# Performance work log

Measured on AMD Instinct MI355X. Metric: run time of the kernel, lower is better.

The kernel has to match this reference:

```python
import jax, jax.numpy as jnp
import numpy as np

H = 256   # hidden_size
B = 64    # batch_size
LP = 2048 # passage length
LQ = 64   # question length


def _linear(x, W, b):
    # torch nn.Linear: y = x @ W.T + b
    return jnp.matmul(x, W.T) + b


def _gru_cell(x, h, w_ih, w_hh, b_ih, b_hh):
    # torch GRUCell semantics: x is input, h is hidden state
    gi = jnp.matmul(x, w_ih.T) + b_ih   # [B, 3*2H]
    gh = jnp.matmul(h, w_hh.T) + b_hh
    i_r, i_z, i_n = jnp.split(gi, 3, axis=-1)
    h_r, h_z, h_n = jnp.split(gh, 3, axis=-1)
    r = jax.nn.sigmoid(i_r + h_r)
    z = jax.nn.sigmoid(i_z + h_z)
    n = jnp.tanh(i_n + r * h_n)
    return (1.0 - z) * n + z * h


def setup_inputs() -> dict:
    key = jax.random.key(0)
    ks = jax.random.split(key, 17)
    s = lambda i, shape: jax.random.normal(ks[i], shape, dtype=jnp.float32) * 0.05
    return {
        "passEnc": jax.random.normal(ks[0], (LP, B, 2 * H), dtype=jnp.float32),
        "quesEnc": jax.random.normal(ks[1], (LQ, B, 2 * H), dtype=jnp.float32),
        "WQu_W": s(2, (H, 2 * H)), "WQu_b": s(3, (H,)),
        "WQv_W": s(4, (H, H)),     "WQv_b": s(5, (H,)),
        "WPh_W": s(6, (H, 2 * H)), "WPh_b": s(7, (H,)),
        "Wah_W": s(8, (H, 2 * H)), "Wah_b": s(9, (H,)),
        "Vt1": s(10, (B, H, 1)),
        "Vt2": s(11, (B, H, 1)),
        "VQr": s(12, (1, 1, H)),
        "gru_wih": s(13, (6 * H, 2 * H)), "gru_whh": s(14, (6 * H, 2 * H)),
        "gru_bih": s(15, (6 * H,)),       "gru_bhh": s(16, (6 * H,)),
    }


def reference(passEnc, quesEnc, WQu_W, WQu_b, WQv_W, WQv_b, WPh_W, WPh_b,
              Wah_W, Wah_b, Vt1, Vt2, VQr, gru_wih, gru_whh, gru_bih, gru_bhh):
    # --- question-aware initial state rQ ---
    # temp: [lQ, B, H] (VQr path broadcasts over lQ and B)
    temp = jnp.tanh(_linear(quesEnc, WQu_W, WQu_b) + _linear(VQr, WQv_W, WQv_b))
    sQ = jnp.einsum('qbh,bh->bq', temp, Vt1[..., 0])          # [B, lQ]
    a = jax.nn.softmax(sQ, axis=1)
    rQ = jnp.einsum('bq,qbd->bd', a, quesEnc)                 # [B, 2H]

    passP = _linear(passEnc, WPh_W, WPh_b)                    # [lP, B, H], reused both steps

    def pointer_step(rQ):
        temp2 = jnp.tanh(passP + _linear(rQ, Wah_W, Wah_b))   # [lP, B, H]
        sP = jnp.einsum('pbh,bh->bp', temp2, Vt2[..., 0])     # [B, lP]
        aP = jax.nn.softmax(sP, axis=1)
        ct = jnp.einsum('bp,pbd->bd', aP, passEnc)            # [B, 2H]
        return aP, ct

    aP1, ct = pointer_step(rQ)
    rQ = _gru_cell(rQ, ct, gru_wih, gru_whh, gru_bih, gru_bhh)
    aP2, _ = pointer_step(rQ)
    return (aP1, aP2)


if __name__ == "__main__":
    out = reference(**setup_inputs())
    print(out[0].shape, out[1].shape)
```

## Files before the change

kernel.cpp:

```cpp
#include <hip/hip_runtime.h>
#include <math.h>


constexpr int Bn   = 64;
constexpr int Hn   = 256;
constexpr int D2H  = 512;
constexpr int LPn  = 2048;
constexpr int LQn  = 64;

typedef __attribute__((ext_vector_type(8))) short bf16x8;
typedef __attribute__((ext_vector_type(4))) float f32x4;
typedef __attribute__((ext_vector_type(4))) short short4v;

__device__ inline float waveAllSum(float v) {
  #pragma unroll
  for (int o = 32; o > 0; o >>= 1) v += __shfl_xor(v, o, 64);
  return v;
}
__device__ inline float waveAllMax(float v) {
  #pragma unroll
  for (int o = 32; o > 0; o >>= 1) v = fmaxf(v, __shfl_xor(v, o, 64));
  return v;
}

__device__ inline short f2bf(float f) {
  union { float f; unsigned u; } v; v.f = f;
  unsigned r = v.u + 0x7FFF + ((v.u >> 16) & 1);
  return (short)(r >> 16);
}

__global__ __launch_bounds__(256) void k_wcvt(const float* __restrict__ WQu,
                                              const float* __restrict__ WPh,
                                              short* __restrict__ wqu16,
                                              short* __restrict__ wph16) {
  int e = (blockIdx.x * 256 + threadIdx.x) * 4;
  const float* src; short* dst; int off;
  if (e < 131072) { src = WQu; dst = wqu16; off = e; }
  else            { src = WPh; dst = wph16; off = e - 131072; }
  f32x4 f = *(const f32x4*)&src[off];
  short4v h;
  h[0] = f2bf(f[0]); h[1] = f2bf(f[1]); h[2] = f2bf(f[2]); h[3] = f2bf(f[3]);
  *(short4v*)&dst[off] = h;
}

__global__ __launch_bounds__(256) void k_v2(const float* __restrict__ VQr,
                                            const float* __restrict__ WQv_W,
                                            const float* __restrict__ WQv_b,
                                            float* __restrict__ v2) {
  __shared__ float s[256];
  int t = threadIdx.x;
  s[t] = VQr[t];
  __syncthreads();
  float acc = WQv_b[t];
  for (int k = 0; k < 256; ++k) acc += s[k] * WQv_W[t * 256 + k];
  v2[t] = acc;
}

__global__ __launch_bounds__(256) void k_mfma_fused(
    const float* __restrict__ A,
    const short* __restrict__ Wb,
    const float* __restrict__ bias,
    const float* __restrict__ u,
    const float* __restrict__ vt,
    float* __restrict__ C,
    float* __restrict__ sOut,
    int ustride, int sstride)
{
  __shared__ __align__(16) short Abuf[64 * 72];
  __shared__ __align__(16) short Bbuf[256 * 72];
  __shared__ float sred[4][64];

  const int tid  = threadIdx.x;
  const int w    = tid >> 6;
  const int l    = tid & 63;
  const int l15  = l & 15;
  const int quad = l >> 4;
  const long bm  = (long)blockIdx.x * 64;

  f32x4 acc[4][4];
  #pragma unroll
  for (int i = 0; i < 4; ++i)
    #pragma unroll
    for (int j = 0; j < 4; ++j)
      acc[i][j] = (f32x4)0.f;

  for (int k0 = 0; k0 < 512; k0 += 64) {
    {
      const int r  = tid >> 2;
      const int ks = (tid & 3) * 16;
      const f32x4* src = (const f32x4*)&A[(bm + r) * 512 + k0 + ks];
      f32x4 f0 = src[0], f1 = src[1], f2 = src[2], f3 = src[3];
      bf16x8 h0, h1;
      h0[0] = f2bf(f0[0]); h0[1] = f2bf(f0[1]); h0[2] = f2bf(f0[2]); h0[3] = f2bf(f0[3]);
      h0[4] = f2bf(f1[0]); h0[5] = f2bf(f1[1]); h0[6] = f2bf(f1[2]); h0[7] = f2bf(f1[3]);
      h1[0] = f2bf(f2[0]); h1[1] = f2bf(f2[1]); h1[2] = f2bf(f2[2]); h1[3] = f2bf(f2[3]);
      h1[4] = f2bf(f3[0]); h1[5] = f2bf(f3[1]); h1[6] = f2bf(f3[2]); h1[7] = f2bf(f3[3]);
      *(bf16x8*)&Abuf[r * 72 + ks]     = h0;
      *(bf16x8*)&Abuf[r * 72 + ks + 8] = h1;
    }
    #pragma unroll
    for (int q = 0; q < 8; ++q) {
      int n = q * 32 + (tid >> 3);
      int s = tid & 7;
      bf16x8 vsh = *(const bf16x8*)&Wb[n * 512 + k0 + s * 8];
      *(bf16x8*)&Bbuf[n * 72 + s * 8] = vsh;
    }
    __syncthreads();
    #pragma unroll
    for (int h = 0; h < 2; ++h) {
      bf16x8 af[4], bfr[4];
      #pragma unroll
      for (int i = 0; i < 4; ++i)
        af[i] = *(const bf16x8*)&Abuf[(i * 16 + l15) * 72 + h * 32 + quad * 8];
      #pragma unroll
      for (int j = 0; j < 4; ++j)
        bfr[j] = *(const bf16x8*)&Bbuf[(w * 64 + j * 16 + l15) * 72 + h * 32 + quad * 8];
      #pragma unroll
      for (int i = 0; i < 4; ++i)
        #pragma unroll
        for (int j = 0; j < 4; ++j)
          acc[i][j] = __builtin_amdgcn_mfma_f32_16x16x32_bf16(af[i], bfr[j], acc[i][j], 0, 0, 0);
    }
    __syncthreads();
  }

  float srow[4][4];
  #pragma unroll
  for (int i = 0; i < 4; ++i) {
    #pragma unroll
    for (int r = 0; r < 4; ++r) {
      const int row = i * 16 + quad * 4 + r;
      float s_acc = 0.f;
      #pragma unroll
      for (int j = 0; j < 4; ++j) {
        const int n = w * 64 + j * 16 + l15;
        float val = acc[i][j][r] + bias[n];
        if (C) C[(bm + row) * 256 + n] = val;
        float uu = u[ustride * row + n];
        s_acc += tanhf(val + uu) * vt[row * 256 + n];
      }
      srow[i][r] = s_acc;
    }
  }
  #pragma unroll
  for (int off = 1; off < 16; off <<= 1) {
    #pragma unroll
    for (int i = 0; i < 4; ++i)
      #pragma unroll
      for (int r = 0; r < 4; ++r)
        srow[i][r] += __shfl_xor(srow[i][r], off, 64);
  }
  if (l15 == 0) {
    #pragma unroll
    for (int i = 0; i < 4; ++i)
      #pragma unroll
      for (int r = 0; r < 4; ++r)
        sred[w][i * 16 + quad * 4 + r] = srow[i][r];
  }
  __syncthreads();
  if (tid < 64) {
    float s = sred[0][tid] + sred[1][tid] + sred[2][tid] + sred[3][tid];
    sOut[(long)tid * sstride + blockIdx.x] = s;
  }
}

constexpr int TM = 64, TN = 64, TK = 32;
constexpr int PAD = 4;

__global__ __launch_bounds__(256) void k_gemm(const float* __restrict__ A,
                                              const float* __restrict__ W,
                                              const float* __restrict__ bias,
                                              float* __restrict__ C,
                                              int M, int N, int K) {
  __shared__ float As[TK][TM + PAD];
  __shared__ float Bs[TK][TN + PAD];
  const int bm = blockIdx.x * TM;
  const int bn = blockIdx.y * TN;
  const int tid = threadIdx.x;
  const int tx = tid & 15;
  const int ty = tid >> 4;
  float acc[4][4] = {};

  for (int k0 = 0; k0 < K; k0 += TK) {
    #pragma unroll
    for (int i = 0; i < 2; ++i) {
      int f = tid + 256 * i;
      int m = f >> 3;
      int kq = (f & 7) << 2;
      float4 v = *(const float4*)&A[(size_t)(bm + m) * K + k0 + kq];
      As[kq + 0][m] = v.x; As[kq + 1][m] = v.y; As[kq + 2][m] = v.z; As[kq + 3][m] = v.w;
    }
    #pragma unroll
    for (int i = 0; i < 2; ++i) {
      int f = tid + 256 * i;
      int n = f >> 3;
      int kq = (f & 7) << 2;
      float4 v = *(const float4*)&W[(size_t)(bn + n) * K + k0 + kq];
      Bs[kq + 0][n] = v.x; Bs[kq + 1][n] = v.y; Bs[kq + 2][n] = v.z; Bs[kq + 3][n] = v.w;
    }
    __syncthreads();
    #pragma unroll
    for (int k = 0; k < TK; ++k) {
      float4 a4 = *(const float4*)&As[k][ty * 4];
      float4 b4 = *(const float4*)&Bs[k][tx * 4];
      float aa[4] = {a4.x, a4.y, a4.z, a4.w};
      float bb[4] = {b4.x, b4.y, b4.z, b4.w};
      #pragma unroll
      for (int i = 0; i < 4; ++i)
        #pragma unroll
        for (int j = 0; j < 4; ++j)
          acc[i][j] = fmaf(aa[i], bb[j], acc[i][j]);
    }
    __syncthreads();
  }

  float4 bset = *(const float4*)&bias[bn + tx * 4];
  #pragma unroll
  for (int i = 0; i < 4; ++i) {
    int m = bm + ty * 4 + i;
    float4 v;
    v.x = acc[i][0] + bset.x;
    v.y = acc[i][1] + bset.y;
    v.z = acc[i][2] + bset.z;
    v.w = acc[i][3] + bset.w;
    *(float4*)&C[(size_t)m * N + bn + tx * 4] = v;
  }
}

__global__ __launch_bounds__(256) void k_softmax_rq(const float* __restrict__ sQ,
                                                    const float* __restrict__ quesEnc,
                                                    float* __restrict__ rQ) {
  int b = blockIdx.x, tid = threadIdx.x;
  __shared__ float s_a[LQn];
  if (tid < 64) {
    float s = sQ[b * LQn + tid];
    float m = waveAllMax(s);
    float e = expf(s - m);
    float sum = waveAllSum(e);
    s_a[tid] = e / sum;
  }
  __syncthreads();
  #pragma unroll
  for (int rep = 0; rep < 2; ++rep) {
    int d = tid + rep * 256;
    float acc = 0.f;
    for (int q = 0; q < LQn; ++q)
      acc += s_a[q] * quesEnc[(size_t)(q * Bn + b) * D2H + d];
    rQ[b * D2H + d] = acc;
  }
}

__global__ __launch_bounds__(256) void k_sp(const float* __restrict__ passP,
                                            const float* __restrict__ u,
                                            const float* __restrict__ Vt2,
                                            float* __restrict__ sP) {
  int flat = blockIdx.x * 4 + (threadIdx.x >> 6);
  int lane = threadIdx.x & 63;
  int b = flat & (Bn - 1);
  int p = flat >> 6;
  float4 v  = *(const float4*)&passP[(size_t)flat * Hn + lane * 4];
  float4 uu = *(const float4*)&u[b * Hn + lane * 4];
  float4 vt = *(const float4*)&Vt2[b * Hn + lane * 4];
  float s = tanhf(v.x + uu.x) * vt.x + tanhf(v.y + uu.y) * vt.y +
            tanhf(v.z + uu.z) * vt.z + tanhf(v.w + uu.w) * vt.w;
  s = waveAllSum(s);
  if (lane == 0) sP[b * LPn + p] = s;
}

__global__ __launch_bounds__(256) void k_softmax(const float* __restrict__ sP,
                                                 float* __restrict__ out) {
  int b = blockIdx.x, tid = threadIdx.x;
  int lane = tid & 63, wid = tid >> 6;
  __shared__ float red[4];
  float v[8];
  float m = -1e30f;
  #pragma unroll
  for (int i = 0; i < 8; ++i) {
    v[i] = sP[b * LPn + i * 256 + tid];
    m = fmaxf(m, v[i]);
  }
  m = waveAllMax(m);
  if (lane == 0) red[wid] = m;
  __syncthreads();
  m = fmaxf(fmaxf(red[0], red[1]), fmaxf(red[2], red[3]));
  float s = 0.f;
  #pragma unroll
  for (int i = 0; i < 8; ++i) { v[i] = expf(v[i] - m); s += v[i]; }
  s = waveAllSum(s);
  __syncthreads();
  if (lane == 0) red[wid] = s;
  __syncthreads();
  s = red[0] + red[1] + red[2] + red[3];
  float inv = 1.0f / s;
  #pragma unroll
  for (int i = 0; i < 8; ++i) out[b * LPn + i * 256 + tid] = v[i] * inv;
}

__global__ __launch_bounds__(256) void k_ct(const float* __restrict__ aP,
                                            const float* __restrict__ passEnc,
                                            float* __restrict__ ct) {
  int b = blockIdx.x;
  int p0 = blockIdx.y * 64;
  int tid = threadIdx.x;
  float acc0 = 0.f, acc1 = 0.f;
  for (int pp = 0; pp < 64; ++pp) {
    int p = p0 + pp;
    float a = aP[b * LPn + p];
    const float* row = &passEnc[(size_t)(p * Bn + b) * D2H];
    acc0 += a * row[tid];
    acc1 += a * row[tid + 256];
  }
  atomicAdd(&ct[b * D2H + tid], acc0);
  atomicAdd(&ct[b * D2H + tid + 256], acc1);
}

__global__ __launch_bounds__(256) void k_gates(const float* __restrict__ gi,
                                               const float* __restrict__ gh,
                                               const float* __restrict__ ct,
                                               float* __restrict__ rQ2) {
  int idx = blockIdx.x * 256 + threadIdx.x;
  int b = idx >> 9;
  int j = idx & 511;
  const float* gib = gi + b * 1536;
  const float* ghb = gh + b * 1536;
  float r = 1.f / (1.f + expf(-(gib[j] + ghb[j])));
  float z = 1.f / (1.f + expf(-(gib[512 + j] + ghb[512 + j])));
  float n = tanhf(gib[1024 + j] + r * ghb[1024 + j]);
  rQ2[b * D2H + j] = (1.f - z) * n + z * ct[b * D2H + j];
}

extern "C" void kernel_launch(void* const* d_in, const int* in_sizes, int n_in,
                              void* d_out, int out_size, void* d_ws, size_t ws_size,
                              hipStream_t stream) {
  const float* passEnc  = (const float*)d_in[0];
  const float* quesEnc  = (const float*)d_in[1];
  const float* WQu_W    = (const float*)d_in[2];
  const float* WQu_b    = (const float*)d_in[3];
  const float* WQv_W    = (const float*)d_in[4];
  const float* WQv_b    = (const float*)d_in[5];
  const float* WPh_W    = (const float*)d_in[6];
  const float* WPh_b    = (const float*)d_in[7];
  const float* Wah_W    = (const float*)d_in[8];
  const float* Wah_b    = (const float*)d_in[9];
  const float* Vt1      = (const float*)d_in[10];
  const float* Vt2      = (const float*)d_in[11];
  const float* VQr      = (const float*)d_in[12];
  const float* gru_wih  = (const float*)d_in[13];
  const float* gru_whh  = (const float*)d_in[14];
  const float* gru_bih  = (const float*)d_in[15];
  const float* gru_bhh  = (const float*)d_in[16];
  float* out = (float*)d_out;

  float* ws = (float*)d_ws;
  float* passP = ws;
  float* v2    = ws + 33554432;
  float* rQ    = v2 + 256;
  float* u1    = rQ + 32768;
  float* u2    = u1 + 16384;
  float* sP    = u2 + 16384;
  float* ct    = sP + 131072;
  float* gi    = ct + 32768;
  float* gh    = gi + 98304;
  float* rQ2   = gh + 98304;
  float* sQ    = rQ2 + 32768;
  short* wqu16 = (short*)(sQ + 4096);
  short* wph16 = wqu16 + 131072;

  k_wcvt<<<256, 256, 0, stream>>>(WQu_W, WPh_W, wqu16, wph16);

  k_v2<<<1, 256, 0, stream>>>(VQr, WQv_W, WQv_b, v2);
  k_mfma_fused<<<LQn, 256, 0, stream>>>(quesEnc, wqu16, WQu_b, v2, Vt1,
                                        nullptr, sQ, 0, LQn);
  k_softmax_rq<<<Bn, 256, 0, stream>>>(sQ, quesEnc, rQ);
  k_gemm<<<dim3(1, Hn / TN), 256, 0, stream>>>(rQ, Wah_W, Wah_b, u1, Bn, Hn, D2H);

  k_mfma_fused<<<LPn, 256, 0, stream>>>(passEnc, wph16, WPh_b, u1, Vt2,
                                        passP, sP, Hn, LPn);
  k_softmax<<<Bn, 256, 0, stream>>>(sP, out);

  hipMemsetAsync(ct, 0, Bn * D2H * sizeof(float), stream);
  k_ct<<<dim3(Bn, LPn / 64), 256, 0, stream>>>(out, passEnc, ct);

  k_gemm<<<dim3(1, 1536 / TN), 256, 0, stream>>>(rQ, gru_wih, gru_bih, gi, Bn, 1536, D2H);
  k_gemm<<<dim3(1, 1536 / TN), 256, 0, stream>>>(ct, gru_whh, gru_bhh, gh, Bn, 1536, D2H);
  k_gates<<<Bn * D2H / 256, 256, 0, stream>>>(gi, gh, ct, rQ2);

  k_gemm<<<dim3(1, Hn / TN), 256, 0, stream>>>(rQ2, Wah_W, Wah_b, u2, Bn, Hn, D2H);
  k_sp<<<LPn * Bn / 4, 256, 0, stream>>>(passP, u2, Vt2, sP);
  k_softmax<<<Bn, 256, 0, stream>>>(sP, out + Bn * LPn);
}
```

Measured before the change: 907.0 us.

## Pre-swizzle weights for direct MFMA loads, fuse GRU and small GEMMs, vectorize ct

Weights are converted into an MFMA-fragment-ordered bf16 layout so the main fused GEMM reads A and B operands straight from global memory into registers, with no LDS staging or barriers, and runs at a 3-waves occupancy hint. The rQ softmax is fused with the u1 projection, and the two GRU GEMMs are fused with the gates into one kernel. A separate small GEMV kernel computes u2. The ct reduction is vectorized with fewer atomics. This removes several launches and LDS traffic, at the cost of uncoalesced-per-row GEMV weight reads and of losing LDS reuse of A and B in the big GEMM.

```diff
diff --git a/kernel.cpp b/kernel.cpp
--- a/kernel.cpp
+++ b/kernel.cpp
@@ -10,7 +10,6 @@
 
 typedef __attribute__((ext_vector_type(8))) short bf16x8;
 typedef __attribute__((ext_vector_type(4))) float f32x4;
-typedef __attribute__((ext_vector_type(4))) short short4v;
 
 __device__ inline float waveAllSum(float v) {
   #pragma unroll
@@ -23,24 +22,49 @@
   return v;
 }
 
-__device__ inline short f2bf(float f) {
+__device__ inline short f2bf_rtne(float f) {
   union { float f; unsigned u; } v; v.f = f;
   unsigned r = v.u + 0x7FFF + ((v.u >> 16) & 1);
   return (short)(r >> 16);
 }
 
+__device__ inline unsigned pk2(float lo, float hi) {
+  union { float f; unsigned u; } a, b; a.f = lo; b.f = hi;
+  return __builtin_amdgcn_perm(b.u + 0x8000u, a.u + 0x8000u, 0x07060302u);
+}
+__device__ inline bf16x8 cvt8(f32x4 a0, f32x4 a1) {
+  union { unsigned u[4]; bf16x8 v; } r;
+  r.u[0] = pk2(a0[0], a0[1]);
+  r.u[1] = pk2(a0[2], a0[3]);
+  r.u[2] = pk2(a1[0], a1[1]);
+  r.u[3] = pk2(a1[2], a1[3]);
+  return r.v;
+}
+
 __global__ __launch_bounds__(256) void k_wcvt(const float* __restrict__ WQu,
                                               const float* __restrict__ WPh,
-                                              short* __restrict__ wqu16,
-                                              short* __restrict__ wph16) {
-  int e = (blockIdx.x * 256 + threadIdx.x) * 4;
-  const float* src; short* dst; int off;
-  if (e < 131072) { src = WQu; dst = wqu16; off = e; }
-  else            { src = WPh; dst = wph16; off = e - 131072; }
-  f32x4 f = *(const f32x4*)&src[off];
-  short4v h;
-  h[0] = f2bf(f[0]); h[1] = f2bf(f[1]); h[2] = f2bf(f[2]); h[3] = f2bf(f[3]);
-  *(short4v*)&dst[off] = h;
+                                              short* __restrict__ q2,
+                                              short* __restrict__ p2) {
+  int s = blockIdx.x * 256 + threadIdx.x;
+  const float* W; short* D; int slot;
+  if (s < 16384) { W = WQu; D = q2; slot = s; }
+  else           { W = WPh; D = p2; slot = s - 16384; }
+  int l    = slot & 63;
+  int rest = slot >> 6;
+  int h    = rest & 1;
+  int k0i  = (rest >> 1) & 7;
+  int wj   = rest >> 4;
+  int l15  = l & 15, quad = l >> 4;
+  int n = (wj >> 2) * 64 + (wj & 3) * 16 + l15;
+  int k = k0i * 64 + h * 32 + quad * 8;
+  f32x4 f0 = *(const f32x4*)&W[n * 512 + k];
+  f32x4 f1 = *(const f32x4*)&W[n * 512 + k + 4];
+  bf16x8 o;
+  o[0] = f2bf_rtne(f0[0]); o[1] = f2bf_rtne(f0[1]);
+  o[2] = f2bf_rtne(f0[2]); o[3] = f2bf_rtne(f0[3]);
+  o[4] = f2bf_rtne(f1[0]); o[5] = f2bf_rtne(f1[1]);
+  o[6] = f2bf_rtne(f1[2]); o[7] = f2bf_rtne(f1[3]);
+  *(bf16x8*)&D[slot * 8] = o;
 }
 
 __global__ __launch_bounds__(256) void k_v2(const float* __restrict__ VQr,
@@ -56,9 +80,9 @@
   v2[t] = acc;
 }
 
-__global__ __launch_bounds__(256) void k_mfma_fused(
+__global__ __launch_bounds__(256, 3) void k_mfma_fused(
     const float* __restrict__ A,
-    const short* __restrict__ Wb,
+    const short* __restrict__ Wb2,
     const float* __restrict__ bias,
     const float* __restrict__ u,
     const float* __restrict__ vt,
@@ -66,10 +90,7 @@
     float* __restrict__ sOut,
     int ustride, int sstride)
 {
-  __shared__ __align__(16) short Abuf[64 * 72];
-  __shared__ __align__(16) short Bbuf[256 * 72];
   __shared__ float sred[4][64];
-
   const int tid  = threadIdx.x;
   const int w    = tid >> 6;
   const int l    = tid & 63;
@@ -84,44 +105,40 @@
     for (int j = 0; j < 4; ++j)
       acc[i][j] = (f32x4)0.f;
 
-  for (int k0 = 0; k0 < 512; k0 += 64) {
-    {
-      const int r  = tid >> 2;
-      const int ks = (tid & 3) * 16;
-      const f32x4* src = (const f32x4*)&A[(bm + r) * 512 + k0 + ks];
-      f32x4 f0 = src[0], f1 = src[1], f2 = src[2], f3 = src[3];
-      bf16x8 h0, h1;
-      h0[0] = f2bf(f0[0]); h0[1] = f2bf(f0[1]); h0[2] = f2bf(f0[2]); h0[3] = f2bf(f0[3]);
-      h0[4] = f2bf(f1[0]); h0[5] = f2bf(f1[1]); h0[6] = f2bf(f1[2]); h0[7] = f2bf(f1[3]);
-      h1[0] = f2bf(f2[0]); h1[1] = f2bf(f2[1]); h1[2] = f2bf(f2[2]); h1[3] = f2bf(f2[3]);
-      h1[4] = f2bf(f3[0]); h1[5] = f2bf(f3[1]); h1[6] = f2bf(f3[2]); h1[7] = f2bf(f3[3]);
-      *(bf16x8*)&Abuf[r * 72 + ks]     = h0;
-      *(bf16x8*)&Abuf[r * 72 + ks + 8] = h1;
-    }
-    #pragma unroll
-    for (int q = 0; q < 8; ++q) {
-      int n = q * 32 + (tid >> 3);
-      int s = tid & 7;
-      bf16x8 vsh = *(const bf16x8*)&Wb[n * 512 + k0 + s * 8];
-      *(bf16x8*)&Bbuf[n * 72 + s * 8] = vsh;
-    }
-    __syncthreads();
+  const float* arow[4];
+  #pragma unroll
+  for (int i = 0; i < 4; ++i)
+    arow[i] = A + (size_t)(bm + i * 16 + l15) * 512 + quad * 8;
+  const short* bptr = Wb2 + (size_t)w * 4 * 8192 + l * 8;
+
+  for (int k0i = 0; k0i < 8; ++k0i) {
+    const int k0 = k0i * 64;
+    f32x4 a0[4][2], a1[4][2];
+    #pragma unroll
+    for (int i = 0; i < 4; ++i)
+      #pragma unroll
+      for (int h = 0; h < 2; ++h) {
+        const float* p = arow[i] + k0 + h * 32;
+        a0[i][h] = *(const f32x4*)p;
+        a1[i][h] = *(const f32x4*)(p + 4);
+      }
+    bf16x8 bfr[2][4];
+    #pragma unroll
+    for (int h = 0; h < 2; ++h)
+      #pragma unroll
+      for (int j = 0; j < 4; ++j)
+        bfr[h][j] = *(const bf16x8*)(bptr + j * 8192 + k0i * 1024 + h * 512);
     #pragma unroll
     for (int h = 0; h < 2; ++h) {
-      bf16x8 af[4], bfr[4];
-      #pragma unroll
-      for (int i = 0; i < 4; ++i)
-        af[i] = *(const bf16x8*)&Abuf[(i * 16 + l15) * 72 + h * 32 + quad * 8];
-      #pragma unroll
-      for (int j = 0; j < 4; ++j)
-        bfr[j] = *(const bf16x8*)&Bbuf[(w * 64 + j * 16 + l15) * 72 + h * 32 + quad * 8];
+      bf16x8 af[4];
+      #pragma unroll
+      for (int i = 0; i < 4; ++i) af[i] = cvt8(a0[i][h], a1[i][h]);
       #pragma unroll
       for (int i = 0; i < 4; ++i)
         #pragma unroll
         for (int j = 0; j < 4; ++j)
-          acc[i][j] = __builtin_amdgcn_mfma_f32_16x16x32_bf16(af[i], bfr[j], acc[i][j], 0, 0, 0);
+          acc[i][j] = __builtin_amdgcn_mfma_f32_16x16x32_bf16(af[i], bfr[h][j], acc[i][j], 0, 0, 0);
     }
-    __syncthreads();
   }
 
   float srow[4][4];
@@ -136,102 +153,39 @@
         const int n = w * 64 + j * 16 + l15;
         float val = acc[i][j][r] + bias[n];
         if (C) C[(bm + row) * 256 + n] = val;
-        float uu = u[ustride * row + n];
-        s_acc += tanhf(val + uu) * vt[row * 256 + n];
+        s_acc += tanhf(val + u[ustride * row + n]) * vt[row * 256 + n];
       }
       srow[i][r] = s_acc;
     }
   }
   #pragma unroll
-  for (int off = 1; off < 16; off <<= 1) {
+  for (int off = 1; off < 16; off <<= 1)
     #pragma unroll
     for (int i = 0; i < 4; ++i)
       #pragma unroll
       for (int r = 0; r < 4; ++r)
         srow[i][r] += __shfl_xor(srow[i][r], off, 64);
-  }
-  if (l15 == 0) {
+  if (l15 == 0)
     #pragma unroll
     for (int i = 0; i < 4; ++i)
       #pragma unroll
       for (int r = 0; r < 4; ++r)
         sred[w][i * 16 + quad * 4 + r] = srow[i][r];
-  }
-  __syncthreads();
-  if (tid < 64) {
-    float s = sred[0][tid] + sred[1][tid] + sred[2][tid] + sred[3][tid];
-    sOut[(long)tid * sstride + blockIdx.x] = s;
-  }
-}
-
-constexpr int TM = 64, TN = 64, TK = 32;
-constexpr int PAD = 4;
-
-__global__ __launch_bounds__(256) void k_gemm(const float* __restrict__ A,
-                                              const float* __restrict__ W,
-                                              const float* __restrict__ bias,
-                                              float* __restrict__ C,
-                                              int M, int N, int K) {
-  __shared__ float As[TK][TM + PAD];
-  __shared__ float Bs[TK][TN + PAD];
-  const int bm = blockIdx.x * TM;
-  const int bn = blockIdx.y * TN;
-  const int tid = threadIdx.x;
-  const int tx = tid & 15;
-  const int ty = tid >> 4;
-  float acc[4][4] = {};
-
-  for (int k0 = 0; k0 < K; k0 += TK) {
-    #pragma unroll
-    for (int i = 0; i < 2; ++i) {
-      int f = tid + 256 * i;
-      int m = f >> 3;
-      int kq = (f & 7) << 2;
-      float4 v = *(const float4*)&A[(size_t)(bm + m) * K + k0 + kq];
-      As[kq + 0][m] = v.x; As[kq + 1][m] = v.y; As[kq + 2][m] = v.z; As[kq + 3][m] = v.w;
-    }
-    #pragma unroll
-    for (int i = 0; i < 2; ++i) {
-      int f = tid + 256 * i;
-      int n = f >> 3;
-      int kq = (f & 7) << 2;
-      float4 v = *(const float4*)&W[(size_t)(bn + n) * K + k0 + kq];
-      Bs[kq + 0][n] = v.x; Bs[kq + 1][n] = v.y; Bs[kq + 2][n] = v.z; Bs[kq + 3][n] = v.w;
-    }
-    __syncthreads();
-    #pragma unroll
-    for (int k = 0; k < TK; ++k) {
-      float4 a4 = *(const float4*)&As[k][ty * 4];
-      float4 b4 = *(const float4*)&Bs[k][tx * 4];
-      float aa[4] = {a4.x, a4.y, a4.z, a4.w};
-      float bb[4] = {b4.x, b4.y, b4.z, b4.w};
-      #pragma unroll
-      for (int i = 0; i < 4; ++i)
-        #pragma unroll
-        for (int j = 0; j < 4; ++j)
-          acc[i][j] = fmaf(aa[i], bb[j], acc[i][j]);
-    }
-    __syncthreads();
-  }
-
-  float4 bset = *(const float4*)&bias[bn + tx * 4];
-  #pragma unroll
-  for (int i = 0; i < 4; ++i) {
-    int m = bm + ty * 4 + i;
-    float4 v;
-    v.x = acc[i][0] + bset.x;
-    v.y = acc[i][1] + bset.y;
-    v.z = acc[i][2] + bset.z;
-    v.w = acc[i][3] + bset.w;
-    *(float4*)&C[(size_t)m * N + bn + tx * 4] = v;
-  }
-}
-
-__global__ __launch_bounds__(256) void k_softmax_rq(const float* __restrict__ sQ,
-                                                    const float* __restrict__ quesEnc,
-                                                    float* __restrict__ rQ) {
+  __syncthreads();
+  if (tid < 64)
+    sOut[(size_t)tid * sstride + blockIdx.x] =
+        sred[0][tid] + sred[1][tid] + sred[2][tid] + sred[3][tid];
+}
+
+__global__ __launch_bounds__(256) void k_rq_u1(const float* __restrict__ sQ,
+                                               const float* __restrict__ quesEnc,
+                                               const float* __restrict__ Wah,
+                                               const float* __restrict__ Wah_b,
+                                               float* __restrict__ rQ,
+                                               float* __restrict__ u1) {
   int b = blockIdx.x, tid = threadIdx.x;
   __shared__ float s_a[LQn];
+  __shared__ float s_r[D2H];
   if (tid < 64) {
     float s = sQ[b * LQn + tid];
     float m = waveAllMax(s);
@@ -246,8 +200,18 @@
     float acc = 0.f;
     for (int q = 0; q < LQn; ++q)
       acc += s_a[q] * quesEnc[(size_t)(q * Bn + b) * D2H + d];
+    s_r[d] = acc;
     rQ[b * D2H + d] = acc;
   }
+  __syncthreads();
+  float accu = Wah_b[tid];
+  const float* wr = Wah + (size_t)tid * 512;
+  for (int k4 = 0; k4 < 128; ++k4) {
+    f32x4 wv = *(const f32x4*)&wr[k4 * 4];
+    f32x4 rv = *(const f32x4*)&s_r[k4 * 4];
+    accu += wv[0] * rv[0] + wv[1] * rv[1] + wv[2] * rv[2] + wv[3] * rv[3];
+  }
+  u1[b * Hn + tid] = accu;
 }
 
 __global__ __launch_bounds__(256) void k_sp(const float* __restrict__ passP,
@@ -299,34 +263,89 @@
 __global__ __launch_bounds__(256) void k_ct(const float* __restrict__ aP,
                                             const float* __restrict__ passEnc,
                                             float* __restrict__ ct) {
-  int b = blockIdx.x;
-  int p0 = blockIdx.y * 64;
-  int tid = threadIdx.x;
-  float acc0 = 0.f, acc1 = 0.f;
+  int b = blockIdx.x, pc = blockIdx.y, tid = threadIdx.x;
+  int dg = tid & 127;
+  int pg = tid >> 7;
+  f32x4 acc = (f32x4)0.f;
   for (int pp = 0; pp < 64; ++pp) {
-    int p = p0 + pp;
+    int p = pc * 128 + pg * 64 + pp;
     float a = aP[b * LPn + p];
-    const float* row = &passEnc[(size_t)(p * Bn + b) * D2H];
-    acc0 += a * row[tid];
-    acc1 += a * row[tid + 256];
-  }
-  atomicAdd(&ct[b * D2H + tid], acc0);
-  atomicAdd(&ct[b * D2H + tid + 256], acc1);
-}
-
-__global__ __launch_bounds__(256) void k_gates(const float* __restrict__ gi,
-                                               const float* __restrict__ gh,
-                                               const float* __restrict__ ct,
-                                               float* __restrict__ rQ2) {
-  int idx = blockIdx.x * 256 + threadIdx.x;
-  int b = idx >> 9;
-  int j = idx & 511;
-  const float* gib = gi + b * 1536;
-  const float* ghb = gh + b * 1536;
-  float r = 1.f / (1.f + expf(-(gib[j] + ghb[j])));
-  float z = 1.f / (1.f + expf(-(gib[512 + j] + ghb[512 + j])));
-  float n = tanhf(gib[1024 + j] + r * ghb[1024 + j]);
-  rQ2[b * D2H + j] = (1.f - z) * n + z * ct[b * D2H + j];
+    acc += a * *(const f32x4*)&passEnc[((size_t)p * Bn + b) * D2H + dg * 4];
+  }
+  __shared__ f32x4 sacc[256];
+  sacc[tid] = acc;
+  __syncthreads();
+  if (pg == 0) {
+    acc += sacc[tid + 128];
+    float* dst = &ct[b * D2H + dg * 4];
+    atomicAdd(dst + 0, acc[0]);
+    atomicAdd(dst + 1, acc[1]);
+    atomicAdd(dst + 2, acc[2]);
+    atomicAdd(dst + 3, acc[3]);
+  }
+}
+
+__global__ __launch_bounds__(256) void k_gru(const float* __restrict__ rQ,
+                                             const float* __restrict__ ct,
+                                             const float* __restrict__ wih,
+                                             const float* __restrict__ whh,
+                                             const float* __restrict__ bih,
+                                             const float* __restrict__ bhh,
+                                             float* __restrict__ rQ2) {
+  int m = blockIdx.x;
+  int j = blockIdx.y * 256 + threadIdx.x;
+  __shared__ float sx[D2H], sh[D2H];
+  sx[threadIdx.x]       = rQ[m * D2H + threadIdx.x];
+  sx[threadIdx.x + 256] = rQ[m * D2H + threadIdx.x + 256];
+  sh[threadIdx.x]       = ct[m * D2H + threadIdx.x];
+  sh[threadIdx.x + 256] = ct[m * D2H + threadIdx.x + 256];
+  __syncthreads();
+  float gr = bih[j], gz = bih[512 + j], gn = bih[1024 + j];
+  float hr = bhh[j], hz = bhh[512 + j], hn = bhh[1024 + j];
+  const float* wr0 = wih + (size_t)j * 512;
+  const float* wr1 = wih + (size_t)(512 + j) * 512;
+  const float* wr2 = wih + (size_t)(1024 + j) * 512;
+  const float* vr0 = whh + (size_t)j * 512;
+  const float* vr1 = whh + (size_t)(512 + j) * 512;
+  const float* vr2 = whh + (size_t)(1024 + j) * 512;
+  for (int k4 = 0; k4 < 128; ++k4) {
+    f32x4 x = *(const f32x4*)&sx[k4 * 4];
+    f32x4 h = *(const f32x4*)&sh[k4 * 4];
+    f32x4 w0 = *(const f32x4*)&wr0[k4 * 4];
+    f32x4 w1 = *(const f32x4*)&wr1[k4 * 4];
+    f32x4 w2 = *(const f32x4*)&wr2[k4 * 4];
+    f32x4 v0 = *(const f32x4*)&vr0[k4 * 4];
+    f32x4 v1 = *(const f32x4*)&vr1[k4 * 4];
+    f32x4 v2 = *(const f32x4*)&vr2[k4 * 4];
+    #pragma unroll
+    for (int e = 0; e < 4; ++e) {
+      gr += w0[e] * x[e]; gz += w1[e] * x[e]; gn += w2[e] * x[e];
+      hr += v0[e] * h[e]; hz += v1[e] * h[e]; hn += v2[e] * h[e];
+    }
+  }
+  float r = 1.f / (1.f + expf(-(gr + hr)));
+  float z = 1.f / (1.f + expf(-(gz + hz)));
+  float nn = tanhf(gn + r * hn);
+  rQ2[m * D2H + j] = (1.f - z) * nn + z * sh[j];
+}
+
+__global__ __launch_bounds__(256) void k_u2(const float* __restrict__ rQ2,
+                                            const float* __restrict__ Wah,
+                                            const float* __restrict__ Wah_b,
+                                            float* __restrict__ u2) {
+  int m = blockIdx.x, n = threadIdx.x;
+  __shared__ float s_r[D2H];
+  s_r[n]       = rQ2[m * D2H + n];
+  s_r[n + 256] = rQ2[m * D2H + n + 256];
+  __syncthreads();
+  float acc = Wah_b[n];
+  const float* wr = Wah + (size_t)n * 512;
+  for (int k4 = 0; k4 < 128; ++k4) {
+    f32x4 wv = *(const f32x4*)&wr[k4 * 4];
+    f32x4 rv = *(const f32x4*)&s_r[k4 * 4];
+    acc += wv[0] * rv[0] + wv[1] * rv[1] + wv[2] * rv[2] + wv[3] * rv[3];
+  }
+  u2[m * Hn + n] = acc;
 }
 
 extern "C" void kernel_launch(void* const* d_in, const int* in_sizes, int n_in,
@@ -359,33 +378,29 @@
   float* u2    = u1 + 16384;
   float* sP    = u2 + 16384;
   float* ct    = sP + 131072;
-  float* gi    = ct + 32768;
-  float* gh    = gi + 98304;
-  float* rQ2   = gh + 98304;
+  float* rQ2   = ct + 32768;
   float* sQ    = rQ2 + 32768;
-  short* wqu16 = (short*)(sQ + 4096);
-  short* wph16 = wqu16 + 131072;
-
-  k_wcvt<<<256, 256, 0, stream>>>(WQu_W, WPh_W, wqu16, wph16);
-
+  short* wqu2  = (short*)(sQ + 4096);
+  short* wph2  = wqu2 + 131072;
+
+  k_wcvt<<<128, 256, 0, stream>>>(WQu_W, WPh_W, wqu2, wph2);
   k_v2<<<1, 256, 0, stream>>>(VQr, WQv_W, WQv_b, v2);
-  k_mfma_fused<<<LQn, 256, 0, stream>>>(quesEnc, wqu16, WQu_b, v2, Vt1,
+
+  k_mfma_fused<<<LQn, 256, 0, stream>>>(quesEnc, wqu2, WQu_b, v2, Vt1,
                                         nullptr, sQ, 0, LQn);
-  k_softmax_rq<<<Bn, 256, 0, stream>>>(sQ, quesEnc, rQ);
-  k_gemm<<<dim3(1, Hn / TN), 256, 0, stream>>>(rQ, Wah_W, Wah_b, u1, Bn, Hn, D2H);
-
-  k_mfma_fused<<<LPn, 256, 0, stream>>>(passEnc, wph16, WPh_b, u1, Vt2,
+  k_rq_u1<<<Bn, 256, 0, stream>>>(sQ, quesEnc, Wah_W, Wah_b, rQ, u1);
+
+  k_mfma_fused<<<LPn, 256, 0, stream>>>(passEnc, wph2, WPh_b, u1, Vt2,
                                         passP, sP, Hn, LPn);
   k_softmax<<<Bn, 256, 0, stream>>>(sP, out);
 
   hipMemsetAsync(ct, 0, Bn * D2H * sizeof(float), stream);
-  k_ct<<<dim3(Bn, LPn / 64), 256, 0, stream>>>(out, passEnc, ct);
-
-  k_gemm<<<dim3(1, 1536 / TN), 256, 0, stream>>>(rQ, gru_wih, gru_bih, gi, Bn, 1536, D2H);
-  k_gemm<<<dim3(1, 1536 / TN), 256, 0, stream>>>(ct, gru_whh, gru_bhh, gh, Bn, 1536, D2H);
-  k_gates<<<Bn * D2H / 256, 256, 0, stream>>>(gi, gh, ct, rQ2);
-
-  k_gemm<<<dim3(1, Hn / TN), 256, 0, stream>>>(rQ2, Wah_W, Wah_b, u2, Bn, Hn, D2H);
+  k_ct<<<dim3(Bn, 16), 256, 0, stream>>>(out, passEnc, ct);
+
+  k_gru<<<dim3(Bn, 2), 256, 0, stream>>>(rQ, ct, gru_wih, gru_whh,
+                                         gru_bih, gru_bhh, rQ2);
+  k_u2<<<Bn, 256, 0, stream>>>(rQ2, Wah_W, Wah_b, u2);
+
   k_sp<<<LPn * Bn / 4, 256, 0, stream>>>(passP, u2, Vt2, sP);
   k_softmax<<<Bn, 256, 0, stream>>>(sP, out + Bn * LPn);
 }
```

Result: no change. 924.0 us (+1.9%).
